# Optimization experiments

Measured on AMD Instinct MI355X. Metric: run time of the kernel, lower is better.

The kernel has to match this reference:

```python
import jax, jax.numpy as jnp
import numpy as np

B, T, D = 2, 2048, 1024
E, H, K = 8, 2048, 2  # n_experts, expert_dim, n_active_experts


def setup_inputs() -> dict:
    key = jax.random.key(0)
    ks = jax.random.split(key, 5)
    s = 0.02
    return {
        "x": jax.random.normal(ks[0], (B, T, D), dtype=jnp.float32),
        "gate_w": jax.random.normal(ks[1], (E, D), dtype=jnp.float32) * s,
        "w1": jax.random.normal(ks[2], (E, H, D), dtype=jnp.float32) * s,
        "w2": jax.random.normal(ks[3], (E, D, H), dtype=jnp.float32) * s,
        "w3": jax.random.normal(ks[4], (E, H, D), dtype=jnp.float32) * s,
    }


def reference(x, gate_w, w1, w2, w3):
    Bb, Tt, Dd = x.shape
    xf = x.reshape(-1, Dd)                       # [N, D]
    logits = xf @ gate_w.T                       # [N, E]
    probs = jax.nn.softmax(logits, axis=-1)
    vals, idx = jax.lax.top_k(probs, K)          # [N, K]
    w = vals / (vals.sum(-1, keepdims=True) + 1e-8)
    onehot = jax.nn.one_hot(idx, E, dtype=xf.dtype)  # [N, K, E]
    comb = jnp.einsum('nk,nke->ne', w, onehot)   # per-token per-expert combine weight
    # Dense expert eval (same math as masked loop): SwiGLU per expert
    h = jnp.einsum('nd,ehd->neh', xf, w1)        # [N, E, H]
    g = jnp.einsum('nd,ehd->neh', xf, w3)
    eo = jnp.einsum('neh,edh->ned', jax.nn.silu(h) * g, w2)  # [N, E, D]
    out = jnp.einsum('ned,ne->nd', eo, comb)
    return out.reshape(Bb, Tt, Dd)
```

## Files before the change

### kernel.cpp

```cpp
#include <hip/hip_runtime.h>
#include <stdint.h>

#define N_TOK 4096
#define DIM   1024
#define NEXP  8
#define HDIM  2048
#define NSLOT 8192

typedef __attribute__((ext_vector_type(8))) short  short8;
typedef __attribute__((ext_vector_type(4))) float  f32x4;

__device__ inline unsigned short f2bf(float f) {
  union { float f; uint32_t u; } v; v.f = f;
  uint32_t u = v.u;
  u += 0x7fffu + ((u >> 16) & 1u);
  return (unsigned short)(u >> 16);
}

__device__ inline void gload_lds16(const void* g, void* l) {
  __builtin_amdgcn_global_load_lds(
      (const __attribute__((address_space(1))) uint32_t*)g,
      (__attribute__((address_space(3))) uint32_t*)l, 16, 0, 0);
}

__global__ __launch_bounds__(256) void cvt_kernel(const float* __restrict__ s,
                                                  unsigned short* __restrict__ d,
                                                  int n4) {
  int i = blockIdx.x * blockDim.x + threadIdx.x;
  int stride = gridDim.x * blockDim.x;
  for (; i < n4; i += stride) {
    float4 f = reinterpret_cast<const float4*>(s)[i];
    ushort4 o;
    o.x = f2bf(f.x); o.y = f2bf(f.y); o.z = f2bf(f.z); o.w = f2bf(f.w);
    reinterpret_cast<ushort4*>(d)[i] = o;
  }
}

__global__ __launch_bounds__(256) void gate_kernel(const float* __restrict__ x,
                                                   const float* __restrict__ gw,
                                                   int* __restrict__ tok_e,
                                                   float* __restrict__ tok_w) {
  __shared__ float gws[NEXP * DIM];
  int tid = threadIdx.x;
  for (int i = tid; i < NEXP * DIM; i += 256) gws[i] = gw[i];
  __syncthreads();
  int lane = tid & 63;
  int token = blockIdx.x * 4 + (tid >> 6);
  const float* xr = x + (size_t)token * DIM;
  float acc[NEXP];
#pragma unroll
  for (int e = 0; e < NEXP; ++e) acc[e] = 0.f;
  for (int i = 0; i < DIM / 64; ++i) {
    float xv = xr[i * 64 + lane];
#pragma unroll
    for (int e = 0; e < NEXP; ++e) acc[e] += xv * gws[e * DIM + i * 64 + lane];
  }
#pragma unroll
  for (int off = 32; off > 0; off >>= 1) {
#pragma unroll
    for (int e = 0; e < NEXP; ++e) acc[e] += __shfl_xor(acc[e], off);
  }
  if (lane == 0) {
    float m = acc[0];
#pragma unroll
    for (int e = 1; e < NEXP; ++e) m = fmaxf(m, acc[e]);
    float ex[NEXP], Z = 0.f;
#pragma unroll
    for (int e = 0; e < NEXP; ++e) { ex[e] = expf(acc[e] - m); Z += ex[e]; }
    int b0 = 0; float v0 = ex[0];
#pragma unroll
    for (int e = 1; e < NEXP; ++e) if (ex[e] > v0) { v0 = ex[e]; b0 = e; }
    int b1 = -1; float v1 = -1.f;
#pragma unroll
    for (int e = 0; e < NEXP; ++e) if (e != b0 && ex[e] > v1) { v1 = ex[e]; b1 = e; }
    float p0 = v0 / Z, p1 = v1 / Z;
    float s = p0 + p1 + 1e-8f;
    tok_e[token * 2 + 0] = b0; tok_e[token * 2 + 1] = b1;
    tok_w[token * 2 + 0] = p0 / s; tok_w[token * 2 + 1] = p1 / s;
  }
}

__global__ __launch_bounds__(1024) void route_kernel(const int* __restrict__ tok_e,
                                                     const float* __restrict__ tok_w,
                                                     int* __restrict__ slot_tok,
                                                     float* __restrict__ slot_w,
                                                     int* __restrict__ cnt_g,
                                                     int* __restrict__ offs_g) {
  __shared__ int cnt[NEXP], offs[NEXP], cur[NEXP];
  int tid = threadIdx.x;
  if (tid < NEXP) cnt[tid] = 0;
  __syncthreads();
  for (int n = tid; n < N_TOK; n += 1024) {
    atomicAdd(&cnt[tok_e[2 * n]], 1);
    atomicAdd(&cnt[tok_e[2 * n + 1]], 1);
  }
  __syncthreads();
  if (tid == 0) {
    int o = 0;
    for (int e = 0; e < NEXP; ++e) { offs[e] = o; cur[e] = o; o += cnt[e]; }
    for (int e = 0; e < NEXP; ++e) { cnt_g[e] = cnt[e]; offs_g[e] = offs[e]; }
  }
  __syncthreads();
  for (int n = tid; n < N_TOK; n += 1024) {
#pragma unroll
    for (int k = 0; k < 2; ++k) {
      int e = tok_e[2 * n + k];
      int p = atomicAdd(&cur[e], 1);
      slot_tok[p] = n;
      slot_w[p] = tok_w[2 * n + k];
    }
  }
}

__global__ __launch_bounds__(512, 2) void gemm1_kernel(const unsigned short* __restrict__ xb,
                                                       const unsigned short* __restrict__ w1b,
                                                       const unsigned short* __restrict__ w3b,
                                                       const int* __restrict__ slot_tok,
                                                       const int* __restrict__ cnt_g,
                                                       const int* __restrict__ offs_g,
                                                       unsigned short* __restrict__ hidden) {
  const int ROWT = 16;
  const int COLT = HDIM / 128;
  int bid = blockIdx.x;
  int e  = bid / (ROWT * COLT);
  int rt = (bid / COLT) % ROWT;
  int ct = bid % COLT;
  int cnt = cnt_g[e];
  if (rt * 256 >= cnt) return;
  int rowBase = offs_g[e] + rt * 256;

  __shared__ alignas(16) unsigned short As[2][256 * 64];
  __shared__ alignas(16) unsigned short B1s[2][128 * 64];
  __shared__ alignas(16) unsigned short B3s[2][128 * 64];
  __shared__ int toks[256];

  int tid = threadIdx.x;
  if (tid < 256) {
    int slot = rowBase + tid; if (slot > NSLOT - 1) slot = NSLOT - 1;
    toks[tid] = slot_tok[slot];
  }
  __syncthreads();

  int wave = tid >> 6, lane = tid & 63;
  int wr = (wave >> 1) * 64;
  int wc = (wave & 1) * 64;
  int sub = lane >> 3;
  int swcol = (((lane & 7) ^ sub) << 3);

  const size_t wbase = (size_t)e * HDIM * DIM;
  const unsigned short* aptr[4];
  const unsigned short* b1ptr[2];
  const unsigned short* b3ptr[2];
#pragma unroll
  for (int i = 0; i < 4; ++i) {
    int r = (wave + i * 8) * 8 + sub;
    aptr[i] = xb + (size_t)toks[r] * DIM + swcol;
  }
#pragma unroll
  for (int i = 0; i < 2; ++i) {
    int r = (wave + i * 8) * 8 + sub;
    b1ptr[i] = w1b + wbase + (size_t)(ct * 128 + r) * DIM + swcol;
    b3ptr[i] = w3b + wbase + (size_t)(ct * 128 + r) * DIM + swcol;
  }

  f32x4 hacc[4][4], gacc[4][4];
#pragma unroll
  for (int m = 0; m < 4; ++m)
#pragma unroll
    for (int n = 0; n < 4; ++n) {
      hacc[m][n] = (f32x4){0.f, 0.f, 0.f, 0.f};
      gacc[m][n] = (f32x4){0.f, 0.f, 0.f, 0.f};
    }

  auto stage = [&](int b, int kt) {
    int k0 = kt * 64;
#pragma unroll
    for (int i = 0; i < 4; ++i)
      gload_lds16(aptr[i] + k0, &As[b][(wave + i * 8) * 512]);
#pragma unroll
    for (int i = 0; i < 2; ++i) {
      gload_lds16(b1ptr[i] + k0, &B1s[b][(wave + i * 8) * 512]);
      gload_lds16(b3ptr[i] + k0, &B3s[b][(wave + i * 8) * 512]);
    }
  };

  const int NKT = DIM / 64;
  stage(0, 0);
  asm volatile("s_waitcnt vmcnt(0)" ::: "memory");
  __syncthreads();

  int key = (lane & 7) << 3;
  for (int kt = 0; kt < NKT; ++kt) {
    int cur = kt & 1;
    if (kt + 1 < NKT) stage(cur ^ 1, kt + 1);
#pragma unroll
    for (int ks = 0; ks < 2; ++ks) {
      int kg = ks * 32 + (lane >> 4) * 8;
      int pc = kg ^ key;
      short8 a[4], b1v[4], b3v[4];
#pragma unroll
      for (int m = 0; m < 4; ++m)
        a[m] = *(const short8*)&As[cur][(wr + m * 16 + (lane & 15)) * 64 + pc];
#pragma unroll
      for (int n = 0; n < 4; ++n) {
        b1v[n] = *(const short8*)&B1s[cur][(wc + n * 16 + (lane & 15)) * 64 + pc];
        b3v[n] = *(const short8*)&B3s[cur][(wc + n * 16 + (lane & 15)) * 64 + pc];
      }
#pragma unroll
      for (int m = 0; m < 4; ++m)
#pragma unroll
        for (int n = 0; n < 4; ++n) {
          hacc[m][n] = __builtin_amdgcn_mfma_f32_16x16x32_bf16(a[m], b1v[n], hacc[m][n], 0, 0, 0);
          gacc[m][n] = __builtin_amdgcn_mfma_f32_16x16x32_bf16(a[m], b3v[n], gacc[m][n], 0, 0, 0);
        }
    }
    asm volatile("s_waitcnt vmcnt(0)" ::: "memory");
    __syncthreads();
  }

  int cbase = ct * 128 + wc;
#pragma unroll
  for (int m = 0; m < 4; ++m) {
#pragma unroll
    for (int q = 0; q < 4; ++q) {
      int r = wr + m * 16 + ((lane >> 4) * 4 + q);
      if (rt * 256 + r < cnt) {
        size_t rowoff = (size_t)(rowBase + r) * HDIM + cbase;
#pragma unroll
        for (int n = 0; n < 4; ++n) {
          float h = hacc[m][n][q], g = gacc[m][n][q];
          float val = (h / (1.f + expf(-h))) * g;
          hidden[rowoff + n * 16 + (lane & 15)] = f2bf(val);
        }
      }
    }
  }
}

__global__ __launch_bounds__(256, 2) void gemm2_kernel(const unsigned short* __restrict__ hidden,
                                                       const unsigned short* __restrict__ w2b,
                                                       const int* __restrict__ slot_tok,
                                                       const float* __restrict__ slot_w,
                                                       const int* __restrict__ cnt_g,
                                                       const int* __restrict__ offs_g,
                                                       float* __restrict__ out) {
  const int ROWT = 32;
  const int COLT = DIM / 128;
  int bid = blockIdx.x;
  int e  = bid / (ROWT * COLT);
  int rt = (bid / COLT) % ROWT;
  int ct = bid % COLT;
  int cnt = cnt_g[e];
  if (rt * 128 >= cnt) return;
  int rowBase = offs_g[e] + rt * 128;

  __shared__ alignas(16) unsigned short As[2][128 * 64];
  __shared__ alignas(16) unsigned short Bs[2][128 * 64];
  __shared__ int   toks[128];
  __shared__ float wgt[128];

  int tid = threadIdx.x;
  if (tid < 128) {
    int slot = rowBase + tid; if (slot > NSLOT - 1) slot = NSLOT - 1;
    toks[tid] = slot_tok[slot];
    wgt[tid]  = slot_w[slot];
  }
  __syncthreads();

  int wave = tid >> 6, lane = tid & 63;
  int wr = (wave >> 1) * 64, wc = (wave & 1) * 64;
  int sub = lane >> 3;
  int swcol = (((lane & 7) ^ sub) << 3);

  const size_t w2base = (size_t)e * DIM * HDIM;
  const unsigned short* aptr[4];
  const unsigned short* bptr[4];
#pragma unroll
  for (int i = 0; i < 4; ++i) {
    int r = (wave + i * 4) * 8 + sub;
    int rg = rowBase + r; if (rg > NSLOT - 1) rg = NSLOT - 1;
    aptr[i] = hidden + (size_t)rg * HDIM + swcol;
    bptr[i] = w2b + w2base + (size_t)(ct * 128 + r) * HDIM + swcol;
  }

  f32x4 acc[4][4];
#pragma unroll
  for (int m = 0; m < 4; ++m)
#pragma unroll
    for (int n = 0; n < 4; ++n) acc[m][n] = (f32x4){0.f, 0.f, 0.f, 0.f};

  auto stage = [&](int b, int kt) {
    int k0 = kt * 64;
#pragma unroll
    for (int i = 0; i < 4; ++i) {
      gload_lds16(aptr[i] + k0, &As[b][(wave + i * 4) * 512]);
      gload_lds16(bptr[i] + k0, &Bs[b][(wave + i * 4) * 512]);
    }
  };

  const int NKT = HDIM / 64;
  stage(0, 0);
  asm volatile("s_waitcnt vmcnt(0)" ::: "memory");
  __syncthreads();

  int key = (lane & 7) << 3;
  for (int kt = 0; kt < NKT; ++kt) {
    int cur = kt & 1;
    if (kt + 1 < NKT) stage(cur ^ 1, kt + 1);
#pragma unroll
    for (int ks = 0; ks < 2; ++ks) {
      int kg = ks * 32 + (lane >> 4) * 8;
      int pc = kg ^ key;
      short8 a[4], b[4];
#pragma unroll
      for (int m = 0; m < 4; ++m)
        a[m] = *(const short8*)&As[cur][(wr + m * 16 + (lane & 15)) * 64 + pc];
#pragma unroll
      for (int n = 0; n < 4; ++n)
        b[n] = *(const short8*)&Bs[cur][(wc + n * 16 + (lane & 15)) * 64 + pc];
#pragma unroll
      for (int m = 0; m < 4; ++m)
#pragma unroll
        for (int n = 0; n < 4; ++n)
          acc[m][n] = __builtin_amdgcn_mfma_f32_16x16x32_bf16(a[m], b[n], acc[m][n], 0, 0, 0);
    }
    asm volatile("s_waitcnt vmcnt(0)" ::: "memory");
    __syncthreads();
  }

  int cbase = ct * 128 + wc;
#pragma unroll
  for (int m = 0; m < 4; ++m) {
#pragma unroll
    for (int q = 0; q < 4; ++q) {
      int r = wr + m * 16 + ((lane >> 4) * 4 + q);
      if (rt * 128 + r < cnt) {
        float w = wgt[r];
        float* orow = out + (size_t)toks[r] * DIM + cbase;
#pragma unroll
        for (int n = 0; n < 4; ++n)
          unsafeAtomicAdd(&orow[n * 16 + (lane & 15)], acc[m][n][q] * w);
      }
    }
  }
}

extern "C" void kernel_launch(void* const* d_in, const int* in_sizes, int n_in,
                              void* d_out, int out_size, void* d_ws, size_t ws_size,
                              hipStream_t stream) {
  const float* x  = (const float*)d_in[0];
  const float* gw = (const float*)d_in[1];
  const float* w1 = (const float*)d_in[2];
  const float* w2 = (const float*)d_in[3];
  const float* w3 = (const float*)d_in[4];
  float* out = (float*)d_out;

  uint8_t* ws = (uint8_t*)d_ws;
  size_t off = 0;
  auto alloc = [&](size_t bytes) -> void* {
    void* p = ws + off; off += (bytes + 255) & ~255ull; return p;
  };
  unsigned short* xb     = (unsigned short*)alloc((size_t)N_TOK * DIM * 2);
  unsigned short* w1b    = (unsigned short*)alloc((size_t)NEXP * HDIM * DIM * 2);
  unsigned short* w3b    = (unsigned short*)alloc((size_t)NEXP * HDIM * DIM * 2);
  unsigned short* w2b    = (unsigned short*)alloc((size_t)NEXP * DIM * HDIM * 2);
  unsigned short* hidden = (unsigned short*)alloc((size_t)NSLOT * HDIM * 2);
  int*   tok_e    = (int*)alloc(N_TOK * 2 * 4);
  float* tok_w    = (float*)alloc(N_TOK * 2 * 4);
  int*   slot_tok = (int*)alloc(NSLOT * 4);
  float* slot_w   = (float*)alloc(NSLOT * 4);
  int*   cnt_g    = (int*)alloc(NEXP * 4);
  int*   offs_g   = (int*)alloc(NEXP * 4);

  hipMemsetAsync(d_out, 0, (size_t)out_size * sizeof(float), stream);

  cvt_kernel<<<2048, 256, 0, stream>>>(x,  xb,  N_TOK * DIM / 4);
  cvt_kernel<<<2048, 256, 0, stream>>>(w1, w1b, NEXP * HDIM * DIM / 4);
  cvt_kernel<<<2048, 256, 0, stream>>>(w3, w3b, NEXP * HDIM * DIM / 4);
  cvt_kernel<<<2048, 256, 0, stream>>>(w2, w2b, NEXP * DIM * HDIM / 4);

  gate_kernel<<<N_TOK / 4, 256, 0, stream>>>(x, gw, tok_e, tok_w);
  route_kernel<<<1, 1024, 0, stream>>>(tok_e, tok_w, slot_tok, slot_w, cnt_g, offs_g);
  gemm1_kernel<<<NEXP * 16 * (HDIM / 128), 512, 0, stream>>>(
      xb, w1b, w3b, slot_tok, cnt_g, offs_g, hidden);
  gemm2_kernel<<<NEXP * 32 * (DIM / 128), 256, 0, stream>>>(
      hidden, w2b, slot_tok, slot_w, cnt_g, offs_g, out);
}
```

Before: 464.0 us.

## Interleave async LDS prefetch with MFMA phases and fuse bf16 conversions

Both expert GEMM main loops are restructured so the next-tile global-to-LDS loads are issued in chunks between MFMA groups. Partial vmcnt waits and raw s_barrier calls replace the full drain plus __syncthreads at the end of each k-step, and s_setprio raises wave priority around MFMA blocks. The aim is to overlap memory latency with matrix math and shorten synchronisation stalls. The four separate fp32-to-bf16 conversion launches are also merged into one kernel to cut launch overhead. The hand-counted vmcnt values make correctness depend on the exact order of issued loads.

After: 460.5 us. No clear change (-0.8%).

```diff
diff --git a/kernel.cpp b/kernel.cpp
--- a/kernel.cpp
+++ b/kernel.cpp
@@ -23,16 +23,29 @@
       (__attribute__((address_space(3))) uint32_t*)l, 16, 0, 0);
 }
 
-__global__ __launch_bounds__(256) void cvt_kernel(const float* __restrict__ s,
-                                                  unsigned short* __restrict__ d,
-                                                  int n4) {
+__global__ __launch_bounds__(256) void cvt_all_kernel(const float* __restrict__ x,
+                                                      const float* __restrict__ w1,
+                                                      const float* __restrict__ w2,
+                                                      const float* __restrict__ w3,
+                                                      unsigned short* __restrict__ xb,
+                                                      unsigned short* __restrict__ w1b,
+                                                      unsigned short* __restrict__ w2b,
+                                                      unsigned short* __restrict__ w3b) {
+  const int NX = N_TOK * DIM / 4;
+  const int NW = NEXP * HDIM * DIM / 4;
   int i = blockIdx.x * blockDim.x + threadIdx.x;
   int stride = gridDim.x * blockDim.x;
-  for (; i < n4; i += stride) {
-    float4 f = reinterpret_cast<const float4*>(s)[i];
+  int total = NX + 3 * NW;
+  for (; i < total; i += stride) {
+    const float* s; unsigned short* d; int j;
+    if (i < NX)               { s = x;  d = xb;  j = i; }
+    else if (i < NX + NW)     { s = w1; d = w1b; j = i - NX; }
+    else if (i < NX + 2 * NW) { s = w2; d = w2b; j = i - NX - NW; }
+    else                      { s = w3; d = w3b; j = i - NX - 2 * NW; }
+    float4 f = reinterpret_cast<const float4*>(s)[j];
     ushort4 o;
     o.x = f2bf(f.x); o.y = f2bf(f.y); o.z = f2bf(f.z); o.w = f2bf(f.w);
-    reinterpret_cast<ushort4*>(d)[i] = o;
+    reinterpret_cast<ushort4*>(d)[j] = o;
   }
 }
 
@@ -172,50 +185,108 @@
       gacc[m][n] = (f32x4){0.f, 0.f, 0.f, 0.f};
     }
 
-  auto stage = [&](int b, int kt) {
-    int k0 = kt * 64;
-#pragma unroll
-    for (int i = 0; i < 4; ++i)
-      gload_lds16(aptr[i] + k0, &As[b][(wave + i * 8) * 512]);
-#pragma unroll
-    for (int i = 0; i < 2; ++i) {
-      gload_lds16(b1ptr[i] + k0, &B1s[b][(wave + i * 8) * 512]);
-      gload_lds16(b3ptr[i] + k0, &B3s[b][(wave + i * 8) * 512]);
-    }
-  };
+  gload_lds16(aptr[0], &As[0][(wave + 0) * 512]);
+  gload_lds16(aptr[1], &As[0][(wave + 8) * 512]);
+  gload_lds16(aptr[2], &As[0][(wave + 16) * 512]);
+  gload_lds16(aptr[3], &As[0][(wave + 24) * 512]);
+  gload_lds16(b1ptr[0], &B1s[0][wave * 512]);
+  gload_lds16(b1ptr[1], &B1s[0][(wave + 8) * 512]);
+  gload_lds16(b3ptr[0], &B3s[0][wave * 512]);
+  gload_lds16(b3ptr[1], &B3s[0][(wave + 8) * 512]);
 
   const int NKT = DIM / 64;
-  stage(0, 0);
-  asm volatile("s_waitcnt vmcnt(0)" ::: "memory");
-  __syncthreads();
-
   int key = (lane & 7) << 3;
+  int l15 = lane & 15;
+  int pc0 = ((lane >> 4) * 8) ^ key;
+  int pc1 = (32 + (lane >> 4) * 8) ^ key;
+
   for (int kt = 0; kt < NKT; ++kt) {
-    int cur = kt & 1;
-    if (kt + 1 < NKT) stage(cur ^ 1, kt + 1);
-#pragma unroll
-    for (int ks = 0; ks < 2; ++ks) {
-      int kg = ks * 32 + (lane >> 4) * 8;
-      int pc = kg ^ key;
-      short8 a[4], b1v[4], b3v[4];
-#pragma unroll
-      for (int m = 0; m < 4; ++m)
-        a[m] = *(const short8*)&As[cur][(wr + m * 16 + (lane & 15)) * 64 + pc];
-#pragma unroll
-      for (int n = 0; n < 4; ++n) {
-        b1v[n] = *(const short8*)&B1s[cur][(wc + n * 16 + (lane & 15)) * 64 + pc];
-        b3v[n] = *(const short8*)&B3s[cur][(wc + n * 16 + (lane & 15)) * 64 + pc];
-      }
-#pragma unroll
-      for (int m = 0; m < 4; ++m)
-#pragma unroll
-        for (int n = 0; n < 4; ++n) {
-          hacc[m][n] = __builtin_amdgcn_mfma_f32_16x16x32_bf16(a[m], b1v[n], hacc[m][n], 0, 0, 0);
-          gacc[m][n] = __builtin_amdgcn_mfma_f32_16x16x32_bf16(a[m], b3v[n], gacc[m][n], 0, 0, 0);
-        }
-    }
-    asm volatile("s_waitcnt vmcnt(0)" ::: "memory");
-    __syncthreads();
+    int c = kt & 1;
+    int nk = (kt + 1) * 64;
+    bool pre = (kt + 1 < NKT);
+
+    __builtin_amdgcn_sched_barrier(0);
+    __builtin_amdgcn_s_barrier();
+    __builtin_amdgcn_sched_barrier(0);
+    if (pre) {
+      gload_lds16(aptr[0] + nk, &As[c ^ 1][(wave + 0) * 512]);
+      gload_lds16(aptr[1] + nk, &As[c ^ 1][(wave + 8) * 512]);
+      asm volatile("s_waitcnt vmcnt(4)" ::: "memory");
+    } else {
+      asm volatile("s_waitcnt vmcnt(2)" ::: "memory");
+    }
+    __builtin_amdgcn_sched_barrier(0);
+    __builtin_amdgcn_s_barrier();
+    __builtin_amdgcn_sched_barrier(0);
+
+    short8 a0[4], a1[4], bv[4];
+#pragma unroll
+    for (int m = 0; m < 4; ++m)
+      a0[m] = *(const short8*)&As[c][(wr + m * 16 + l15) * 64 + pc0];
+#pragma unroll
+    for (int n = 0; n < 4; ++n)
+      bv[n] = *(const short8*)&B1s[c][(wc + n * 16 + l15) * 64 + pc0];
+    if (pre) {
+      gload_lds16(aptr[2] + nk, &As[c ^ 1][(wave + 16) * 512]);
+      gload_lds16(aptr[3] + nk, &As[c ^ 1][(wave + 24) * 512]);
+    }
+    __builtin_amdgcn_s_setprio(1);
+#pragma unroll
+    for (int m = 0; m < 4; ++m)
+#pragma unroll
+      for (int n = 0; n < 4; ++n)
+        hacc[m][n] = __builtin_amdgcn_mfma_f32_16x16x32_bf16(a0[m], bv[n], hacc[m][n], 0, 0, 0);
+    __builtin_amdgcn_s_setprio(0);
+
+#pragma unroll
+    for (int m = 0; m < 4; ++m)
+      a1[m] = *(const short8*)&As[c][(wr + m * 16 + l15) * 64 + pc1];
+#pragma unroll
+    for (int n = 0; n < 4; ++n)
+      bv[n] = *(const short8*)&B1s[c][(wc + n * 16 + l15) * 64 + pc1];
+    if (pre) {
+      gload_lds16(b1ptr[0] + nk, &B1s[c ^ 1][wave * 512]);
+      gload_lds16(b1ptr[1] + nk, &B1s[c ^ 1][(wave + 8) * 512]);
+    }
+    __builtin_amdgcn_s_setprio(1);
+#pragma unroll
+    for (int m = 0; m < 4; ++m)
+#pragma unroll
+      for (int n = 0; n < 4; ++n)
+        hacc[m][n] = __builtin_amdgcn_mfma_f32_16x16x32_bf16(a1[m], bv[n], hacc[m][n], 0, 0, 0);
+    __builtin_amdgcn_s_setprio(0);
+
+    if (pre) asm volatile("s_waitcnt vmcnt(6)" ::: "memory");
+    else     asm volatile("s_waitcnt vmcnt(0)" ::: "memory");
+    __builtin_amdgcn_sched_barrier(0);
+    __builtin_amdgcn_s_barrier();
+    __builtin_amdgcn_sched_barrier(0);
+
+#pragma unroll
+    for (int n = 0; n < 4; ++n)
+      bv[n] = *(const short8*)&B3s[c][(wc + n * 16 + l15) * 64 + pc0];
+    if (pre) {
+      gload_lds16(b3ptr[0] + nk, &B3s[c ^ 1][wave * 512]);
+      gload_lds16(b3ptr[1] + nk, &B3s[c ^ 1][(wave + 8) * 512]);
+    }
+    __builtin_amdgcn_s_setprio(1);
+#pragma unroll
+    for (int m = 0; m < 4; ++m)
+#pragma unroll
+      for (int n = 0; n < 4; ++n)
+        gacc[m][n] = __builtin_amdgcn_mfma_f32_16x16x32_bf16(a0[m], bv[n], gacc[m][n], 0, 0, 0);
+    __builtin_amdgcn_s_setprio(0);
+
+#pragma unroll
+    for (int n = 0; n < 4; ++n)
+      bv[n] = *(const short8*)&B3s[c][(wc + n * 16 + l15) * 64 + pc1];
+    __builtin_amdgcn_s_setprio(1);
+#pragma unroll
+    for (int m = 0; m < 4; ++m)
+#pragma unroll
+      for (int n = 0; n < 4; ++n)
+        gacc[m][n] = __builtin_amdgcn_mfma_f32_16x16x32_bf16(a1[m], bv[n], gacc[m][n], 0, 0, 0);
+    __builtin_amdgcn_s_setprio(0);
   }
 
   int cbase = ct * 128 + wc;
@@ -289,43 +360,72 @@
 #pragma unroll
     for (int n = 0; n < 4; ++n) acc[m][n] = (f32x4){0.f, 0.f, 0.f, 0.f};
 
-  auto stage = [&](int b, int kt) {
-    int k0 = kt * 64;
-#pragma unroll
-    for (int i = 0; i < 4; ++i) {
-      gload_lds16(aptr[i] + k0, &As[b][(wave + i * 4) * 512]);
-      gload_lds16(bptr[i] + k0, &Bs[b][(wave + i * 4) * 512]);
-    }
-  };
+#pragma unroll
+  for (int i = 0; i < 4; ++i)
+    gload_lds16(aptr[i], &As[0][(wave + i * 4) * 512]);
+#pragma unroll
+  for (int i = 0; i < 4; ++i)
+    gload_lds16(bptr[i], &Bs[0][(wave + i * 4) * 512]);
 
   const int NKT = HDIM / 64;
-  stage(0, 0);
-  asm volatile("s_waitcnt vmcnt(0)" ::: "memory");
-  __syncthreads();
-
   int key = (lane & 7) << 3;
+  int l15 = lane & 15;
+  int pc0 = ((lane >> 4) * 8) ^ key;
+  int pc1 = (32 + (lane >> 4) * 8) ^ key;
+
   for (int kt = 0; kt < NKT; ++kt) {
-    int cur = kt & 1;
-    if (kt + 1 < NKT) stage(cur ^ 1, kt + 1);
-#pragma unroll
-    for (int ks = 0; ks < 2; ++ks) {
-      int kg = ks * 32 + (lane >> 4) * 8;
-      int pc = kg ^ key;
-      short8 a[4], b[4];
-#pragma unroll
-      for (int m = 0; m < 4; ++m)
-        a[m] = *(const short8*)&As[cur][(wr + m * 16 + (lane & 15)) * 64 + pc];
-#pragma unroll
-      for (int n = 0; n < 4; ++n)
-        b[n] = *(const short8*)&Bs[cur][(wc + n * 16 + (lane & 15)) * 64 + pc];
-#pragma unroll
-      for (int m = 0; m < 4; ++m)
-#pragma unroll
-        for (int n = 0; n < 4; ++n)
-          acc[m][n] = __builtin_amdgcn_mfma_f32_16x16x32_bf16(a[m], b[n], acc[m][n], 0, 0, 0);
-    }
-    asm volatile("s_waitcnt vmcnt(0)" ::: "memory");
-    __syncthreads();
+    int c = kt & 1;
+    int nk = (kt + 1) * 64;
+    bool pre = (kt + 1 < NKT);
+
+    __builtin_amdgcn_sched_barrier(0);
+    __builtin_amdgcn_s_barrier();
+    __builtin_amdgcn_sched_barrier(0);
+    if (pre) {
+#pragma unroll
+      for (int i = 0; i < 4; ++i)
+        gload_lds16(aptr[i] + nk, &As[c ^ 1][(wave + i * 4) * 512]);
+      asm volatile("s_waitcnt vmcnt(4)" ::: "memory");
+    } else {
+      asm volatile("s_waitcnt vmcnt(0)" ::: "memory");
+    }
+    __builtin_amdgcn_sched_barrier(0);
+    __builtin_amdgcn_s_barrier();
+    __builtin_amdgcn_sched_barrier(0);
+
+    short8 a[4], b[4];
+#pragma unroll
+    for (int m = 0; m < 4; ++m)
+      a[m] = *(const short8*)&As[c][(wr + m * 16 + l15) * 64 + pc0];
+#pragma unroll
+    for (int n = 0; n < 4; ++n)
+      b[n] = *(const short8*)&Bs[c][(wc + n * 16 + l15) * 64 + pc0];
+    if (pre) {
+#pragma unroll
+      for (int i = 0; i < 4; ++i)
+        gload_lds16(bptr[i] + nk, &Bs[c ^ 1][(wave + i * 4) * 512]);
+    }
+    __builtin_amdgcn_s_setprio(1);
+#pragma unroll
+    for (int m = 0; m < 4; ++m)
+#pragma unroll
+      for (int n = 0; n < 4; ++n)
+        acc[m][n] = __builtin_amdgcn_mfma_f32_16x16x32_bf16(a[m], b[n], acc[m][n], 0, 0, 0);
+    __builtin_amdgcn_s_setprio(0);
+
+#pragma unroll
+    for (int m = 0; m < 4; ++m)
+      a[m] = *(const short8*)&As[c][(wr + m * 16 + l15) * 64 + pc1];
+#pragma unroll
+    for (int n = 0; n < 4; ++n)
+      b[n] = *(const short8*)&Bs[c][(wc + n * 16 + l15) * 64 + pc1];
+    __builtin_amdgcn_s_setprio(1);
+#pragma unroll
+    for (int m = 0; m < 4; ++m)
+#pragma unroll
+      for (int n = 0; n < 4; ++n)
+        acc[m][n] = __builtin_amdgcn_mfma_f32_16x16x32_bf16(a[m], b[n], acc[m][n], 0, 0, 0);
+    __builtin_amdgcn_s_setprio(0);
   }
 
   int cbase = ct * 128 + wc;
@@ -374,10 +474,7 @@
 
   hipMemsetAsync(d_out, 0, (size_t)out_size * sizeof(float), stream);
 
-  cvt_kernel<<<2048, 256, 0, stream>>>(x,  xb,  N_TOK * DIM / 4);
-  cvt_kernel<<<2048, 256, 0, stream>>>(w1, w1b, NEXP * HDIM * DIM / 4);
-  cvt_kernel<<<2048, 256, 0, stream>>>(w3, w3b, NEXP * HDIM * DIM / 4);
-  cvt_kernel<<<2048, 256, 0, stream>>>(w2, w2b, NEXP * DIM * HDIM / 4);
+  cvt_all_kernel<<<2048, 256, 0, stream>>>(x, w1, w2, w3, xb, w1b, w2b, w3b);
 
   gate_kernel<<<N_TOK / 4, 256, 0, stream>>>(x, gw, tok_e, tok_w);
   route_kernel<<<1, 1024, 0, stream>>>(tok_e, tok_w, slot_tok, slot_w, cnt_g, offs_g);
```
